# Performance work log

Hardware: AMD Instinct MI355X
Metric: run time of the kernel (lower is better)

Reference implementation:

```python
import jax, jax.numpy as jnp
import numpy as np

N_NODES = 100000
IN_DIM = 128
N_EDGES = 600000
HIDDEN = 128


def setup_inputs() -> dict:
    key = jax.random.key(0)
    k_z, k_e, k_w1, k_b1, k_w2, k_b2 = jax.random.split(key, 6)
    z = jax.random.normal(k_z, (N_NODES, IN_DIM), dtype=jnp.float32)
    edge_index = jax.random.randint(k_e, (2, N_EDGES), 0, N_NODES, dtype=jnp.int64)
    # torch.nn.Linear weights: W has shape (out, in), y = x @ W.T + b
    lim1 = 1.0 / np.sqrt(2 * IN_DIM)
    W1 = jax.random.uniform(k_w1, (HIDDEN, 2 * IN_DIM), jnp.float32, -lim1, lim1)
    b1 = jax.random.uniform(k_b1, (HIDDEN,), jnp.float32, -lim1, lim1)
    lim2 = 1.0 / np.sqrt(HIDDEN)
    W2 = jax.random.uniform(k_w2, (1, HIDDEN), jnp.float32, -lim2, lim2)
    b2 = jax.random.uniform(k_b2, (1,), jnp.float32, -lim2, lim2)
    return {"z": z, "edge_index": edge_index, "W1": W1, "b1": b1, "W2": W2, "b2": b2}


def reference(z, edge_index, W1, b1, W2, b2):
    src, dst = edge_index[0], edge_index[1]
    pair = jnp.concatenate([z[src], z[dst]], axis=1)        # [E, 2*in_dim]
    h = jax.nn.relu(pair @ W1.T + b1)                        # [E, 128]
    out = (h @ W2.T + b2).squeeze(-1)                        # [E]
    return out
```

## Files before the change

kernel.cpp:

```cpp
#include <hip/hip_runtime.h>

#define IN_DIM 128
#define NCOL   256

typedef __bf16 bfx8 __attribute__((ext_vector_type(8)));
typedef __bf16 bfx4 __attribute__((ext_vector_type(4)));
typedef float  f32x4 __attribute__((ext_vector_type(4)));

__global__ __launch_bounds__(256, 2) void gemm_mfma(
    const float* __restrict__ z, const float* __restrict__ W1,
    const float* __restrict__ b1, __bf16* __restrict__ UV, int nchunks)
{
    const int tid  = threadIdx.x;
    const int wave = tid >> 6;
    const int lane = tid & 63;
    const int l15  = lane & 15;
    const int q    = lane >> 4;
    const int n0   = wave * 64;

    bfx8  bfrag[4][4];
    f32x4 bias[4];
#pragma unroll
    for (int nt = 0; nt < 4; ++nt) {
        const int n = n0 + nt * 16 + l15;
        const float* src = (n < 128) ? (W1 + (size_t)n * 256)
                                     : (W1 + (size_t)(n - 128) * 256 + 128);
#pragma unroll
        for (int kk = 0; kk < 4; ++kk) {
            float4 f0 = *(const float4*)(src + kk * 32 + q * 8);
            float4 f1 = *(const float4*)(src + kk * 32 + q * 8 + 4);
            bfx8 b;
            b[0]=(__bf16)f0.x; b[1]=(__bf16)f0.y; b[2]=(__bf16)f0.z; b[3]=(__bf16)f0.w;
            b[4]=(__bf16)f1.x; b[5]=(__bf16)f1.y; b[6]=(__bf16)f1.z; b[7]=(__bf16)f1.w;
            bfrag[nt][kk] = b;
        }
        if (n0 + nt * 16 < 128) bias[nt] = *(const f32x4*)(b1 + n0 + nt * 16 + q * 4);
        else                    bias[nt] = (f32x4){0.f, 0.f, 0.f, 0.f};
    }

    for (int c = blockIdx.x; c < nchunks; c += gridDim.x) {
        const int m0 = c * 32;

        bfx8 afrag[2][4];
#pragma unroll
        for (int mt = 0; mt < 2; ++mt)
#pragma unroll
            for (int kk = 0; kk < 4; ++kk) {
                const float* p = z + (size_t)(m0 + mt * 16 + l15) * IN_DIM + kk * 32 + q * 8;
                float4 f0 = *(const float4*)p;
                float4 f1 = *(const float4*)(p + 4);
                bfx8 a;
                a[0]=(__bf16)f0.x; a[1]=(__bf16)f0.y; a[2]=(__bf16)f0.z; a[3]=(__bf16)f0.w;
                a[4]=(__bf16)f1.x; a[5]=(__bf16)f1.y; a[6]=(__bf16)f1.z; a[7]=(__bf16)f1.w;
                afrag[mt][kk] = a;
            }

        f32x4 acc[2][4];
#pragma unroll
        for (int mt = 0; mt < 2; ++mt)
#pragma unroll
            for (int nt = 0; nt < 4; ++nt)
                acc[mt][nt] = (f32x4){0.f, 0.f, 0.f, 0.f};

#pragma unroll
        for (int kk = 0; kk < 4; ++kk)
#pragma unroll
            for (int mt = 0; mt < 2; ++mt)
#pragma unroll
                for (int nt = 0; nt < 4; ++nt)
                    acc[mt][nt] = __builtin_amdgcn_mfma_f32_16x16x32_bf16(
                        bfrag[nt][kk], afrag[mt][kk], acc[mt][nt], 0, 0, 0);

#pragma unroll
        for (int mt = 0; mt < 2; ++mt) {
            __bf16* dst = UV + (size_t)(m0 + mt * 16 + l15) * NCOL + n0 + q * 4;
#pragma unroll
            for (int nt = 0; nt < 4; ++nt) {
                bfx4 v;
#pragma unroll
                for (int r = 0; r < 4; ++r)
                    v[r] = (__bf16)(acc[mt][nt][r] + bias[nt][r]);
                *(bfx4*)(dst + nt * 16) = v;
            }
        }
    }
}

__global__ __launch_bounds__(256) void edge_mlp(
    const __bf16* __restrict__ UV, const int* __restrict__ ei,
    const float* __restrict__ W2, const float* __restrict__ b2,
    float* __restrict__ out, int E)
{
    const int gt   = blockIdx.x * blockDim.x + threadIdx.x;
    const int lane = threadIdx.x & 15;
    const int g    = gt >> 4;
    const int e0   = g * 2;
    const int j0   = lane * 8;

    float ww[8];
    {
        float4 w0 = *(const float4*)(W2 + j0);
        float4 w1 = *(const float4*)(W2 + j0 + 4);
        ww[0] = w0.x; ww[1] = w0.y; ww[2] = w0.z; ww[3] = w0.w;
        ww[4] = w1.x; ww[5] = w1.y; ww[6] = w1.z; ww[7] = w1.w;
    }

    if (e0 >= E) return;

    const int2 srcp = *(const int2*)(ei + e0);
    const int2 dstp = *(const int2*)(ei + E + e0);

    bfx8 u0 = *(const bfx8*)(UV + (size_t)srcp.x * NCOL + j0);
    bfx8 v0 = *(const bfx8*)(UV + (size_t)dstp.x * NCOL + 128 + j0);
    bfx8 u1 = *(const bfx8*)(UV + (size_t)srcp.y * NCOL + j0);
    bfx8 v1 = *(const bfx8*)(UV + (size_t)dstp.y * NCOL + 128 + j0);

    float s0 = 0.f, s1 = 0.f;
#pragma unroll
    for (int i = 0; i < 8; ++i) {
        float h0 = (float)u0[i] + (float)v0[i];
        float h1 = (float)u1[i] + (float)v1[i];
        s0 = fmaf(fmaxf(h0, 0.f), ww[i], s0);
        s1 = fmaf(fmaxf(h1, 0.f), ww[i], s1);
    }

#pragma unroll
    for (int d = 1; d < 16; d <<= 1) {
        s0 += __shfl_xor(s0, d);
        s1 += __shfl_xor(s1, d);
    }

    if (lane == 0) {
        float bb = b2[0];
        *(float2*)(out + e0) = make_float2(s0 + bb, s1 + bb);
    }
}

extern "C" void kernel_launch(void* const* d_in, const int* in_sizes, int n_in,
                              void* d_out, int out_size, void* d_ws, size_t ws_size,
                              hipStream_t stream)
{
    const float* z  = (const float*)d_in[0];
    const int*   ei = (const int*)d_in[1];
    const float* W1 = (const float*)d_in[2];
    const float* b1 = (const float*)d_in[3];
    const float* W2 = (const float*)d_in[4];
    const float* b2 = (const float*)d_in[5];
    float* out = (float*)d_out;

    const int M = in_sizes[0] / IN_DIM;
    const int E = in_sizes[1] / 2;

    __bf16* UV = (__bf16*)d_ws;

    const int nchunks = M / 32;
    gemm_mfma<<<512, 256, 0, stream>>>(z, W1, b1, UV, nchunks);

    int groups  = (E + 1) / 2;
    int eblocks = (groups * 16 + 255) / 256;
    edge_mlp<<<eblocks, 256, 0, stream>>>(UV, ei, W2, b2, out, E);
}
```

Before: 168.3 us.

## Double-buffer z tiles in LDS via async global_load_lds with swizzle

The GEMM kernel now stages each 32-row chunk of z into a double-buffered LDS tile using global_load_lds direct-to-LDS loads, prefetching the next chunk while the current one is computed. Previously every wave loaded the whole A tile redundantly from global memory per chunk. An XOR swizzle is applied to the global source addresses so that LDS reads avoid bank conflicts. This adds 32KB of LDS per block and a barrier per iteration, which may reduce occupancy.

```diff
diff --git a/kernel.cpp b/kernel.cpp
--- a/kernel.cpp
+++ b/kernel.cpp
@@ -7,10 +7,14 @@
 typedef __bf16 bfx4 __attribute__((ext_vector_type(4)));
 typedef float  f32x4 __attribute__((ext_vector_type(4)));
 
+__device__ __forceinline__ int swz(int x) { return x ^ (((x >> 9) & 7) << 4); }
+
 __global__ __launch_bounds__(256, 2) void gemm_mfma(
     const float* __restrict__ z, const float* __restrict__ W1,
     const float* __restrict__ b1, __bf16* __restrict__ UV, int nchunks)
 {
+    __shared__ float abuf[2][32 * IN_DIM];
+
     const int tid  = threadIdx.x;
     const int wave = tid >> 6;
     const int lane = tid & 63;
@@ -38,22 +42,30 @@
         else                    bias[nt] = (f32x4){0.f, 0.f, 0.f, 0.f};
     }
 
-    for (int c = blockIdx.x; c < nchunks; c += gridDim.x) {
+    auto STAGE = [&](int b, int cc) {
+        const char* gbase = (const char*)(z + (size_t)cc * 32 * IN_DIM);
+#pragma unroll
+        for (int i = 0; i < 4; ++i) {
+            const int seg  = (wave * 4 + i) << 10;
+            const int loff = seg + lane * 16;
+            __builtin_amdgcn_global_load_lds(
+                (const __attribute__((address_space(1))) void*)(gbase + swz(loff)),
+                (__attribute__((address_space(3))) void*)((char*)&abuf[b][0] + seg),
+                16, 0, 0);
+        }
+    };
+
+    int c = blockIdx.x;
+    STAGE(0, c);
+    __syncthreads();
+    int cur = 0;
+
+    for (; c < nchunks; c += gridDim.x) {
+        const int cn = c + gridDim.x;
+        if (cn < nchunks) STAGE(cur ^ 1, cn);
+
+        const char* tb = (const char*)&abuf[cur][0];
         const int m0 = c * 32;
-
-        bfx8 afrag[2][4];
-#pragma unroll
-        for (int mt = 0; mt < 2; ++mt)
-#pragma unroll
-            for (int kk = 0; kk < 4; ++kk) {
-                const float* p = z + (size_t)(m0 + mt * 16 + l15) * IN_DIM + kk * 32 + q * 8;
-                float4 f0 = *(const float4*)p;
-                float4 f1 = *(const float4*)(p + 4);
-                bfx8 a;
-                a[0]=(__bf16)f0.x; a[1]=(__bf16)f0.y; a[2]=(__bf16)f0.z; a[3]=(__bf16)f0.w;
-                a[4]=(__bf16)f1.x; a[5]=(__bf16)f1.y; a[6]=(__bf16)f1.z; a[7]=(__bf16)f1.w;
-                afrag[mt][kk] = a;
-            }
 
         f32x4 acc[2][4];
 #pragma unroll
@@ -63,13 +75,26 @@
                 acc[mt][nt] = (f32x4){0.f, 0.f, 0.f, 0.f};
 
 #pragma unroll
-        for (int kk = 0; kk < 4; ++kk)
+        for (int kk = 0; kk < 4; ++kk) {
+            bfx8 af[2];
+#pragma unroll
+            for (int mt = 0; mt < 2; ++mt) {
+                const int r = mt * 16 + l15;
+                const int o = r * 512 + kk * 128 + q * 32;
+                f32x4 f0 = *(const f32x4*)(tb + swz(o));
+                f32x4 f1 = *(const f32x4*)(tb + swz(o + 16));
+                bfx8 a;
+                a[0]=(__bf16)f0[0]; a[1]=(__bf16)f0[1]; a[2]=(__bf16)f0[2]; a[3]=(__bf16)f0[3];
+                a[4]=(__bf16)f1[0]; a[5]=(__bf16)f1[1]; a[6]=(__bf16)f1[2]; a[7]=(__bf16)f1[3];
+                af[mt] = a;
+            }
 #pragma unroll
             for (int mt = 0; mt < 2; ++mt)
 #pragma unroll
                 for (int nt = 0; nt < 4; ++nt)
                     acc[mt][nt] = __builtin_amdgcn_mfma_f32_16x16x32_bf16(
-                        bfrag[nt][kk], afrag[mt][kk], acc[mt][nt], 0, 0, 0);
+                        bfrag[nt][kk], af[mt], acc[mt][nt], 0, 0, 0);
+        }
 
 #pragma unroll
         for (int mt = 0; mt < 2; ++mt) {
@@ -83,6 +108,9 @@
                 *(bfx4*)(dst + nt * 16) = v;
             }
         }
+
+        __syncthreads();
+        cur ^= 1;
     }
 }
 
```

Measured after the change: 154.4 us. 1.09x faster.
